# Optimization experiments

Hardware: AMD Instinct MI355X
Metric: run time of the kernel (lower is better)

The kernel has to match this reference:

```python
import jax, jax.numpy as jnp
import numpy as np

H = 56; W = 56; WS = 7; NW = WS * WS  # 49 tokens per window
HEADS = 8; DIM = 256; HIDDEN = 4 * DIM
SHIFT = NW // 2  # gilbert shift = 24 (shift_size > 0)
SCALE = (DIM // HEADS) ** -0.5
EPS = 1e-5


def _sgn(v):
    return -1 if v < 0 else 1 if v > 0 else 0


def _generate2d(x, y, ax, ay, bx, by, result):
    w = abs(ax + ay); h = abs(bx + by)
    dax, day = _sgn(ax), _sgn(ay); dbx, dby = _sgn(bx), _sgn(by)
    if h == 1 or w == 1:
        if h == 1:
            for _ in range(w):
                result.append((x, y)); x, y = x + dax, y + day
        elif w == 1:
            for _ in range(h):
                result.append((x, y)); x, y = x + dbx, y + dby
        return
    ax2, ay2 = ax // 2, ay // 2; bx2, by2 = bx // 2, by // 2
    w2 = abs(ax2 + ay2); h2 = abs(bx2 + by2)
    if 2 * w > 3 * h:
        if w2 % 2 and w > 2:
            ax2, ay2 = ax2 + dax, ay2 + day
        _generate2d(x, y, ax2, ay2, bx, by, result)
        _generate2d(x + ax2, y + ay2, ax - ax2, ay - ay2, bx, by, result)
    else:
        if h2 % 2 and h > 2:
            bx2, by2 = bx2 + dbx, by2 + dby
        _generate2d(x, y, bx2, by2, ax2, ay2, result)
        _generate2d(x + bx2, y + by2, ax, ay, bx - bx2, by - by2, result)
        _generate2d(x + (ax - dax) + (bx2 - dbx), y + (ay - day) + (by2 - dby),
                    -bx2, -by2, -(ax - ax2), -(ay - ay2), result)


def _gilbert2d(width, height):
    result = []
    if width >= height:
        _generate2d(0, 0, width, 0, 0, height, result)
    else:
        _generate2d(0, 0, 0, height, width, 0, result)
    return result


def _make_rel_index():
    # reverse_map[idx] = (y, x) for gilbert position idx
    path = _gilbert2d(W, H)
    rev = np.zeros((H * W, 2), dtype=np.int64)
    for i, (px, py) in enumerate(path[:H * W]):
        rev[i, 0] = py; rev[i, 1] = px
    pos = np.roll(rev, SHIFT, axis=0)  # shifted block: roll positions by ws^2//2
    n_windows = (H * W) // NW
    pos = pos[:n_windows * NW].reshape(n_windows, NW, 2)
    dh = pos[:, :, 0][:, :, None] - pos[:, :, 0][:, None, :] + (H - 1)
    dw = pos[:, :, 1][:, :, None] - pos[:, :, 1][:, None, :] + (W - 1)
    return (dh * (2 * W - 1) + dw).astype(np.int32)  # (nW, 49, 49)


def setup_inputs() -> dict:
    key = jax.random.key(0)
    ks = jax.random.split(key, 8)
    B, L, C = 32, H * W, DIM
    return {
        "x": jax.random.normal(ks[0], (B, L, C), jnp.float32),
        "qkv_w": jax.random.normal(ks[1], (C, 3 * C), jnp.float32) * 0.02,
        "qkv_b": jnp.zeros((3 * C,), jnp.float32),
        "proj_w": jax.random.normal(ks[2], (C, C), jnp.float32) * 0.02,
        "proj_b": jnp.zeros((C,), jnp.float32),
        "bias_table": jax.random.normal(ks[3], ((2 * H - 1) * (2 * W - 1), HEADS), jnp.float32) * 0.02,
        "norm1_w": jnp.ones((C,), jnp.float32),
        "norm1_b": jnp.zeros((C,), jnp.float32),
        "norm2_w": jnp.ones((C,), jnp.float32),
        "norm2_b": jnp.zeros((C,), jnp.float32),
        "fc1_w": jax.random.normal(ks[4], (C, HIDDEN), jnp.float32) * 0.02,
        "fc1_b": jnp.zeros((HIDDEN,), jnp.float32),
        "fc2_w": jax.random.normal(ks[5], (HIDDEN, C), jnp.float32) * 0.02,
        "fc2_b": jnp.zeros((C,), jnp.float32),
        "rel_index": jnp.asarray(_make_rel_index()),
    }


def _layernorm(x, w, b):
    mu = jnp.mean(x, axis=-1, keepdims=True)
    var = jnp.mean(jnp.square(x - mu), axis=-1, keepdims=True)
    return (x - mu) * jax.lax.rsqrt(var + EPS) * w + b


def reference(x, qkv_w, qkv_b, proj_w, proj_b, bias_table,
              norm1_w, norm1_b, norm2_w, norm2_b,
              fc1_w, fc1_b, fc2_w, fc2_b, rel_index):
    B, L, C = x.shape
    n_win = L // NW
    hd = C // HEADS

    shortcut = x
    h = _layernorm(x, norm1_w, norm1_b)
    # gilbert forward shift along the curve, then window partition
    h = jnp.roll(h, SHIFT, axis=1)
    hw = h.reshape(B * n_win, NW, C)

    qkv = (hw @ qkv_w + qkv_b).reshape(B * n_win, NW, 3, HEADS, hd)
    qkv = jnp.transpose(qkv, (2, 0, 3, 1, 4))  # (3, B*nW, heads, N, hd)
    q, k, v = qkv[0] * SCALE, qkv[1], qkv[2]

    attn = jnp.einsum('bhnd,bhmd->bhnm', q, k)  # (B*nW, heads, 49, 49)
    bias = jnp.transpose(bias_table[rel_index], (0, 3, 1, 2))  # (nW, heads, 49, 49)
    attn = attn.reshape(B, n_win, HEADS, NW, NW) + bias[None]
    attn = jax.nn.softmax(attn, axis=-1).reshape(B * n_win, HEADS, NW, NW)

    out = jnp.einsum('bhnm,bhmd->bhnd', attn, v)
    out = jnp.transpose(out, (0, 2, 1, 3)).reshape(B * n_win, NW, C)
    out = out @ proj_w + proj_b

    # window merge + gilbert reverse shift
    out = out.reshape(B, L, C)
    out = jnp.roll(out, -SHIFT, axis=1)

    x = shortcut + out
    h2 = _layernorm(x, norm2_w, norm2_b)
    h2 = jax.nn.gelu(h2 @ fc1_w + fc1_b, approximate=False) @ fc2_w + fc2_b
    return x + h2
```

## Files before the change

### kernel.cpp

```cpp
#include <hip/hip_runtime.h>
#include <math.h>

typedef unsigned short u16;
typedef __attribute__((ext_vector_type(8))) short bfrag;
typedef __attribute__((ext_vector_type(4))) float f32x4;
typedef __attribute__((ext_vector_type(4))) unsigned short us4;

#define B_SZ 32
#define L_SZ 3136
#define C_SZ 256
#define NHEADS 8
#define HID_SZ 1024
#define NW 49
#define NWIN 64
#define SHIFT 24
#define M_SZ (B_SZ * L_SZ)
#define SCALEF 0.17677669529663687f

__device__ __forceinline__ float bf2f(u16 u) {
  union { unsigned int i; float f; } v; v.i = ((unsigned)u) << 16; return v.f;
}
__device__ __forceinline__ u16 f2bf(float f) {
  union { unsigned int i; float f; } v; v.f = f;
  return (u16)((v.i + 0x7fffu + ((v.i >> 16) & 1u)) >> 16);
}
__device__ __forceinline__ void gload_lds16(const u16* g, u16* l) {
  __builtin_amdgcn_global_load_lds(
      (const __attribute__((address_space(1))) unsigned int*)g,
      (__attribute__((address_space(3))) unsigned int*)l, 16, 0, 0);
}

__global__ void transpose_kernel(const float* __restrict__ in, u16* __restrict__ out,
                                 int K, int N) {
  const int idx = blockIdx.x * 256 + threadIdx.x;
  if (idx >= K * N) return;
  const int n = idx / K;
  const int k = idx - n * K;
  out[idx] = f2bf(in[(size_t)k * N + n]);
}

__global__ void bias_kernel(const float* __restrict__ tab, const int* __restrict__ rel,
                            float* __restrict__ bm) {
  const int idx = blockIdx.x * 256 + threadIdx.x;
  const int tot = NWIN * NHEADS * NW * NW;
  if (idx >= tot) return;
  const int w = idx / (NHEADS * NW * NW);
  const int r = idx - w * (NHEADS * NW * NW);
  const int h = r / (NW * NW);
  const int ij = r - h * (NW * NW);
  bm[idx] = tab[(size_t)rel[w * NW * NW + ij] * NHEADS + h];
}

__global__ __launch_bounds__(256) void ln1_kernel(
    const float* __restrict__ x, const float* __restrict__ w,
    const float* __restrict__ b, u16* __restrict__ out) {
  const int wv = threadIdx.x >> 6;
  const int lane = threadIdx.x & 63;
  const int row0 = blockIdx.x * 16 + wv * 4;
  float4 u[4];
#pragma unroll
  for (int r = 0; r < 4; ++r)
    u[r] = *((const float4*)x + (size_t)(row0 + r) * 64 + lane);
  float s[4], sq[4];
#pragma unroll
  for (int r = 0; r < 4; ++r) {
    s[r]  = u[r].x + u[r].y + u[r].z + u[r].w;
    sq[r] = u[r].x * u[r].x + u[r].y * u[r].y + u[r].z * u[r].z + u[r].w * u[r].w;
  }
#pragma unroll
  for (int d = 1; d < 64; d <<= 1)
#pragma unroll
    for (int r = 0; r < 4; ++r) {
      s[r] += __shfl_xor(s[r], d); sq[r] += __shfl_xor(sq[r], d);
    }
  float wv4[4], bv4[4];
#pragma unroll
  for (int j = 0; j < 4; ++j) { wv4[j] = w[lane * 4 + j]; bv4[j] = b[lane * 4 + j]; }
#pragma unroll
  for (int r = 0; r < 4; ++r) {
    const int row = row0 + r;
    const float mu = s[r] * (1.0f / C_SZ);
    const float rs = rsqrtf(sq[r] * (1.0f / C_SZ) - mu * mu + 1e-5f);
    const int bb = row / L_SZ;
    int l2 = row - bb * L_SZ + SHIFT;
    if (l2 >= L_SZ) l2 -= L_SZ;
    const float vv[4] = {u[r].x, u[r].y, u[r].z, u[r].w};
    us4 ov;
#pragma unroll
    for (int j = 0; j < 4; ++j) ov[j] = f2bf((vv[j] - mu) * rs * wv4[j] + bv4[j]);
    *(us4*)(out + ((size_t)bb * L_SZ + l2) * C_SZ + lane * 4) = ov;
  }
}

__global__ __launch_bounds__(256) void ln2_kernel(
    const u16* __restrict__ x, const float* __restrict__ w,
    const float* __restrict__ b, u16* __restrict__ out) {
  const int wv = threadIdx.x >> 6;
  const int lane = threadIdx.x & 63;
  const int row0 = blockIdx.x * 16 + wv * 4;
  us4 u[4];
#pragma unroll
  for (int r = 0; r < 4; ++r)
    u[r] = *(const us4*)(x + (size_t)(row0 + r) * C_SZ + lane * 4);
  float v[4][4], s[4], sq[4];
#pragma unroll
  for (int r = 0; r < 4; ++r) {
    s[r] = 0.f; sq[r] = 0.f;
#pragma unroll
    for (int j = 0; j < 4; ++j) {
      v[r][j] = bf2f(u[r][j]); s[r] += v[r][j]; sq[r] += v[r][j] * v[r][j];
    }
  }
#pragma unroll
  for (int d = 1; d < 64; d <<= 1)
#pragma unroll
    for (int r = 0; r < 4; ++r) {
      s[r] += __shfl_xor(s[r], d); sq[r] += __shfl_xor(sq[r], d);
    }
  float wv4[4], bv4[4];
#pragma unroll
  for (int j = 0; j < 4; ++j) { wv4[j] = w[lane * 4 + j]; bv4[j] = b[lane * 4 + j]; }
#pragma unroll
  for (int r = 0; r < 4; ++r) {
    const float mu = s[r] * (1.0f / C_SZ);
    const float rs = rsqrtf(sq[r] * (1.0f / C_SZ) - mu * mu + 1e-5f);
    us4 ov;
#pragma unroll
    for (int j = 0; j < 4; ++j) ov[j] = f2bf((v[r][j] - mu) * rs * wv4[j] + bv4[j]);
    *(us4*)(out + (size_t)(row0 + r) * C_SZ + lane * 4) = ov;
  }
}

#define BM 128
#define BN 128
#define BKT 64

template <int MODE>
__global__ __launch_bounds__(256, 4) void gemm_kernel(
    const u16* __restrict__ A, const u16* __restrict__ Bt,
    const float* __restrict__ bias, int N, int K, void* __restrict__ Cout,
    const float* __restrict__ resx, const u16* __restrict__ resb2) {
  __shared__ u16 Als[BM * BKT];
  __shared__ u16 Bls[BN * BKT];
  const int nbx = N / BN;
  const int per = gridDim.x >> 3;
  const int lin = (blockIdx.x & 7) * per + (blockIdx.x >> 3);
  const int by = lin / nbx;
  const int bx = lin - by * nbx;
  const int m0 = by * BM;
  const int n0 = bx * BN;

  const int tid = threadIdx.x;
  const int lane = tid & 63;
  const int lr = lane & 15;
  const int lg = lane >> 4;
  const int wid = tid >> 6;
  const int wm = (wid >> 1) * 64;
  const int wn = (wid & 1) * 64;

  const int grow = lane >> 3;
  const int gch = (lane & 7) ^ grow;

  const f32x4 fzero = {0.f, 0.f, 0.f, 0.f};
  f32x4 acc[4][4];
#pragma unroll
  for (int i = 0; i < 4; ++i)
#pragma unroll
    for (int j = 0; j < 4; ++j) acc[i][j] = fzero;

  const u16* Agl = A + (size_t)m0 * K + gch * 8;
  const u16* Bgl = Bt + (size_t)n0 * K + gch * 8;

  for (int k0 = 0; k0 < K; k0 += BKT) {
#pragma unroll
    for (int g = 0; g < 4; ++g) {
      const int rbase = wid * 32 + g * 8;
      gload_lds16(Agl + (size_t)(rbase + grow) * K + k0, Als + rbase * 64);
      gload_lds16(Bgl + (size_t)(rbase + grow) * K + k0, Bls + rbase * 64);
    }
    __syncthreads();
#pragma unroll
    for (int s = 0; s < 2; ++s) {
      const int kg = s * 4 + lg;
      bfrag af[4], bfv[4];
#pragma unroll
      for (int m = 0; m < 4; ++m) {
        const int r = wm + m * 16 + lr;
        af[m] = *(const bfrag*)(Als + r * 64 + ((kg ^ (r & 7)) * 8));
      }
#pragma unroll
      for (int n = 0; n < 4; ++n) {
        const int r = wn + n * 16 + lr;
        bfv[n] = *(const bfrag*)(Bls + r * 64 + ((kg ^ (r & 7)) * 8));
      }
#pragma unroll
      for (int m = 0; m < 4; ++m)
#pragma unroll
        for (int n = 0; n < 4; ++n)
          acc[m][n] = __builtin_amdgcn_mfma_f32_16x16x32_bf16(af[m], bfv[n],
                                                              acc[m][n], 0, 0, 0);
    }
    __syncthreads();
  }

  float bv4[4];
#pragma unroll
  for (int n = 0; n < 4; ++n) bv4[n] = bias[n0 + wn + n * 16 + lr];

#pragma unroll
  for (int m = 0; m < 4; ++m) {
#pragma unroll
    for (int i = 0; i < 4; ++i) {
      const int row = m0 + wm + m * 16 + lg * 4 + i;
      if (MODE == 1) {
        const int bb = row / L_SZ;
        int l2 = row - bb * L_SZ - SHIFT;
        if (l2 < 0) l2 += L_SZ;
        const size_t orow = (size_t)bb * L_SZ + l2;
#pragma unroll
        for (int n = 0; n < 4; ++n) {
          const int col = n0 + wn + n * 16 + lr;
          ((u16*)Cout)[orow * N + col] =
              f2bf(resx[orow * N + col] + acc[m][n][i] + bv4[n]);
        }
      } else if (MODE == 2) {
#pragma unroll
        for (int n = 0; n < 4; ++n) {
          const int col = n0 + wn + n * 16 + lr;
          float v = acc[m][n][i] + bv4[n];
          v = 0.5f * v * (1.0f + erff(v * 0.70710678f));
          ((u16*)Cout)[(size_t)row * N + col] = f2bf(v);
        }
      } else if (MODE == 3) {
#pragma unroll
        for (int n = 0; n < 4; ++n) {
          const int col = n0 + wn + n * 16 + lr;
          ((float*)Cout)[(size_t)row * N + col] =
              acc[m][n][i] + bv4[n] + bf2f(resb2[(size_t)row * N + col]);
        }
      } else {
#pragma unroll
        for (int n = 0; n < 4; ++n) {
          const int col = n0 + wn + n * 16 + lr;
          ((u16*)Cout)[(size_t)row * N + col] = f2bf(acc[m][n][i] + bv4[n]);
        }
      }
    }
  }
}

__global__ __launch_bounds__(256) void attn_kernel(const u16* __restrict__ qkv,
                                                   const float* __restrict__ bm,
                                                   u16* __restrict__ out, int widx0) {
  __shared__ u16 Pls[4][64 * 72];
  __shared__ u16 Vls[4][64 * 32];
  const int wl = blockIdx.x >> 1;
  const int half = blockIdx.x & 1;
  const int w = (widx0 + wl) & (NWIN - 1);
  const int wv = threadIdx.x >> 6;
  const int lane = threadIdx.x & 63;
  const int lr = lane & 15;
  const int lg = lane >> 4;
  const size_t base = (size_t)wl * NW;
  u16* P = Pls[wv];
  u16* Vl = Vls[wv];
  const f32x4 fzero = {0.f, 0.f, 0.f, 0.f};
  const int h = half * 4 + wv;

#pragma unroll
  for (int g = 0; g < 4; ++g) {
    int row = g * 16 + (lane >> 2);
    if (row > NW - 1) row = NW - 1;
    const int sc = (lane & 3) ^ ((row ^ (row >> 2)) & 3);
    gload_lds16(qkv + (base + row) * 768 + 512 + h * 32 + sc * 8, Vl + g * 512);
  }

  bfrag qf[4], kf[4];
#pragma unroll
  for (int m = 0; m < 4; ++m) {
    int r = m * 16 + lr; if (r > NW - 1) r = NW - 1;
    qf[m] = *(const bfrag*)(qkv + (base + r) * 768 + h * 32 + lg * 8);
    kf[m] = *(const bfrag*)(qkv + (base + r) * 768 + 256 + h * 32 + lg * 8);
  }
  f32x4 s[4][4];
#pragma unroll
  for (int m = 0; m < 4; ++m)
#pragma unroll
    for (int n = 0; n < 4; ++n)
      s[m][n] = __builtin_amdgcn_mfma_f32_16x16x32_bf16(qf[m], kf[n], fzero, 0, 0, 0);

  const float* bh = bm + (size_t)(w * NHEADS + h) * (NW * NW);
#pragma unroll
  for (int m = 0; m < 4; ++m) {
#pragma unroll
    for (int i = 0; i < 4; ++i) {
      const int row = m * 16 + lg * 4 + i;
      const int brow = row > NW - 1 ? NW - 1 : row;
      float vals[4];
#pragma unroll
      for (int n = 0; n < 4; ++n) {
        const int c = n * 16 + lr;
        vals[n] = (c < NW) ? (s[m][n][i] * SCALEF + bh[brow * NW + c]) : -1e30f;
      }
      float mx = fmaxf(fmaxf(vals[0], vals[1]), fmaxf(vals[2], vals[3]));
#pragma unroll
      for (int d = 1; d < 16; d <<= 1) mx = fmaxf(mx, __shfl_xor(mx, d));
      float sum = 0.f;
#pragma unroll
      for (int n = 0; n < 4; ++n) { vals[n] = __expf(vals[n] - mx); sum += vals[n]; }
#pragma unroll
      for (int d = 1; d < 16; d <<= 1) sum += __shfl_xor(sum, d);
      const float inv = 1.0f / sum;
#pragma unroll
      for (int n = 0; n < 4; ++n)
        P[row * 72 + n * 16 + lr] = f2bf(vals[n] * inv);
    }
  }
  asm volatile("s_waitcnt vmcnt(0)" ::: "memory");
  f32x4 o[4][2];
#pragma unroll
  for (int m = 0; m < 4; ++m) { o[m][0] = fzero; o[m][1] = fzero; }
#pragma unroll
  for (int s2 = 0; s2 < 2; ++s2) {
    bfrag pf[4], vf[2];
#pragma unroll
    for (int m = 0; m < 4; ++m)
      pf[m] = *(const bfrag*)(P + (m * 16 + lr) * 72 + s2 * 32 + lg * 8);
#pragma unroll
    for (int n = 0; n < 2; ++n) {
      const int d = n * 16 + lr;
      const int cd = d >> 3;
#pragma unroll
      for (int i = 0; i < 8; ++i) {
        const int kk = s2 * 32 + lg * 8 + i;
        const int slot = cd ^ ((kk ^ (kk >> 2)) & 3);
        vf[n][i] = *(const short*)(Vl + kk * 32 + slot * 8 + (d & 7));
      }
    }
#pragma unroll
    for (int m = 0; m < 4; ++m)
#pragma unroll
      for (int n = 0; n < 2; ++n)
        o[m][n] = __builtin_amdgcn_mfma_f32_16x16x32_bf16(pf[m], vf[n],
                                                          o[m][n], 0, 0, 0);
  }
#pragma unroll
  for (int m = 0; m < 4; ++m)
#pragma unroll
    for (int i = 0; i < 4; ++i) {
      const int row = m * 16 + lg * 4 + i;
      if (row < NW) {
#pragma unroll
        for (int n = 0; n < 2; ++n)
          out[(base + row) * C_SZ + h * 32 + n * 16 + lr] = f2bf(o[m][n][i]);
      }
    }
}

extern "C" void kernel_launch(void* const* d_in, const int* in_sizes, int n_in,
                              void* d_out, int out_size, void* d_ws, size_t ws_size,
                              hipStream_t stream) {
  (void)in_sizes; (void)n_in; (void)out_size;
  const float* x     = (const float*)d_in[0];
  const float* qkvw  = (const float*)d_in[1];
  const float* qkvb  = (const float*)d_in[2];
  const float* projw = (const float*)d_in[3];
  const float* projb = (const float*)d_in[4];
  const float* btab  = (const float*)d_in[5];
  const float* n1w   = (const float*)d_in[6];
  const float* n1b   = (const float*)d_in[7];
  const float* n2w   = (const float*)d_in[8];
  const float* n2b   = (const float*)d_in[9];
  const float* fc1w  = (const float*)d_in[10];
  const float* fc1b  = (const float*)d_in[11];
  const float* fc2w  = (const float*)d_in[12];
  const float* fc2b  = (const float*)d_in[13];
  const int* rel     = (const int*)d_in[14];

  char* ws = (char*)d_ws;
  size_t off = 0;
  auto alloc = [&](size_t bytes) -> char* {
    char* p = ws + off; off += (bytes + 255) & ~(size_t)255; return p;
  };
  u16* qkvwT   = (u16*)alloc((size_t)768 * 256 * 2);
  u16* projwT  = (u16*)alloc((size_t)256 * 256 * 2);
  u16* fc1wT   = (u16*)alloc((size_t)1024 * 256 * 2);
  u16* fc2wT   = (u16*)alloc((size_t)256 * 1024 * 2);
  float* biasm = (float*)alloc((size_t)NWIN * NHEADS * NW * NW * 4);
  u16* bufh    = (u16*)alloc((size_t)M_SZ * C_SZ * 2);
  u16* x2b     = (u16*)alloc((size_t)M_SZ * C_SZ * 2);

  const size_t scr_chunk = (size_t)(M_SZ / 2) * HID_SZ * 2;
  const int nch = (ws_size >= off + scr_chunk) ? 2 : 4;
  const int mch = M_SZ / nch;
  const int wch = (B_SZ * NWIN) / nch;
  char* tail = ws + off;
  u16* qkvbuf   = (u16*)tail;
  u16* scratch2 = (u16*)tail;

  transpose_kernel<<<(256 * 768 + 255) / 256, 256, 0, stream>>>(qkvw, qkvwT, 256, 768);
  transpose_kernel<<<(256 * 256 + 255) / 256, 256, 0, stream>>>(projw, projwT, 256, 256);
  transpose_kernel<<<(256 * 1024 + 255) / 256, 256, 0, stream>>>(fc1w, fc1wT, 256, 1024);
  transpose_kernel<<<(1024 * 256 + 255) / 256, 256, 0, stream>>>(fc2w, fc2wT, 1024, 256);
  bias_kernel<<<(NWIN * NHEADS * NW * NW + 255) / 256, 256, 0, stream>>>(btab, rel, biasm);

  ln1_kernel<<<M_SZ / 16, 256, 0, stream>>>(x, n1w, n1b, bufh);

  for (int c = 0; c < nch; ++c) {
    const size_t roff = (size_t)c * mch;
    gemm_kernel<0><<<(768 / BN) * (mch / BM), 256, 0, stream>>>(
        bufh + roff * C_SZ, qkvwT, qkvb, 768, 256, qkvbuf, nullptr, nullptr);
    attn_kernel<<<wch * 2, 256, 0, stream>>>(qkvbuf, biasm, bufh + roff * C_SZ,
                                             c * wch);
  }

  gemm_kernel<1><<<(256 / BN) * (M_SZ / BM), 256, 0, stream>>>(
      bufh, projwT, projb, 256, 256, x2b, x, nullptr);

  for (int q = 0; q < nch; ++q) {
    const size_t roff = (size_t)q * mch;
    ln2_kernel<<<mch / 16, 256, 0, stream>>>(x2b + roff * C_SZ, n2w, n2b,
                                             bufh + roff * C_SZ);
    gemm_kernel<2><<<(HID_SZ / BN) * (mch / BM), 256, 0, stream>>>(
        bufh + roff * C_SZ, fc1wT, fc1b, 1024, 256, scratch2, nullptr, nullptr);
    gemm_kernel<3><<<(256 / BN) * (mch / BM), 256, 0, stream>>>(
        scratch2, fc2wT, fc2b, 256, 1024, (float*)d_out + roff * C_SZ,
        nullptr, x2b + roff * C_SZ);
  }
}
```

Before: 458.2 us.

## Add double-buffered 256x256-tile GEMM for MLP and process MLP unchunked

Adds a 512-thread GEMM kernel that computes 256x256 output tiles. It double-buffers the A and B tiles in LDS with swizzled direct-to-LDS loads, and is used for the fc1 (GELU) and fc2 (residual) GEMMs. When the workspace can hold the full hidden activation, the MLP now runs as a single chunk rather than two or four, and the QKV/attention loop is fixed at two chunks. The goal is more operand reuse per tile, load latency overlapped with MFMA work, and fewer launches. In exchange the new kernel uses about 128KB of LDS and a large accumulator set, so it fits only one block per CU. The fc2 grid is also small relative to the CU count, which risks tail imbalance.

```diff
diff --git a/kernel.cpp b/kernel.cpp
--- a/kernel.cpp
+++ b/kernel.cpp
@@ -139,7 +139,7 @@
 __global__ __launch_bounds__(256, 4) void gemm_kernel(
     const u16* __restrict__ A, const u16* __restrict__ Bt,
     const float* __restrict__ bias, int N, int K, void* __restrict__ Cout,
-    const float* __restrict__ resx, const u16* __restrict__ resb2) {
+    const float* __restrict__ resx) {
   __shared__ u16 Als[BM * BKT];
   __shared__ u16 Bls[BN * BKT];
   const int nbx = N / BN;
@@ -223,26 +223,120 @@
           ((u16*)Cout)[orow * N + col] =
               f2bf(resx[orow * N + col] + acc[m][n][i] + bv4[n]);
         }
-      } else if (MODE == 2) {
+      } else {
 #pragma unroll
         for (int n = 0; n < 4; ++n) {
           const int col = n0 + wn + n * 16 + lr;
+          ((u16*)Cout)[(size_t)row * N + col] = f2bf(acc[m][n][i] + bv4[n]);
+        }
+      }
+    }
+  }
+}
+
+template <int MODE>
+__global__ __launch_bounds__(512, 2) void gemm256_kernel(
+    const u16* __restrict__ A, const u16* __restrict__ Bt,
+    const float* __restrict__ bias, int N, int K, void* __restrict__ Cout,
+    const u16* __restrict__ resb2) {
+  __shared__ u16 Als[2][256 * 64];
+  __shared__ u16 Bls[2][256 * 64];
+  const int nbx = N / 256;
+  int lin;
+  if ((gridDim.x & 7) == 0) {
+    const int per = gridDim.x >> 3;
+    lin = (blockIdx.x & 7) * per + (blockIdx.x >> 3);
+  } else {
+    lin = blockIdx.x;
+  }
+  const int by = lin / nbx;
+  const int bx = lin - by * nbx;
+  const int m0 = by * 256;
+  const int n0 = bx * 256;
+
+  const int tid = threadIdx.x;
+  const int lane = tid & 63;
+  const int lr = lane & 15;
+  const int lg = lane >> 4;
+  const int wid = tid >> 6;
+  const int wr = wid >> 2;
+  const int wc = wid & 3;
+  const int grow = lane >> 3;
+  const int gch = (lane & 7) ^ grow;
+
+  const f32x4 fzero = {0.f, 0.f, 0.f, 0.f};
+  f32x4 acc[8][4];
+#pragma unroll
+  for (int m = 0; m < 8; ++m)
+#pragma unroll
+    for (int n = 0; n < 4; ++n) acc[m][n] = fzero;
+
+  const u16* Agl = A + (size_t)m0 * K + gch * 8;
+  const u16* Bgl = Bt + (size_t)n0 * K + gch * 8;
+
+  auto stage = [&](int buf, int k0) {
+#pragma unroll
+    for (int g = 0; g < 4; ++g) {
+      const int rb = wid * 32 + g * 8;
+      gload_lds16(Agl + (size_t)(rb + grow) * K + k0, Als[buf] + rb * 64);
+      gload_lds16(Bgl + (size_t)(rb + grow) * K + k0, Bls[buf] + rb * 64);
+    }
+  };
+
+  const int nk = K / 64;
+  stage(0, 0);
+  __syncthreads();
+  int cur = 0;
+  for (int kb = 0; kb < nk; ++kb) {
+    if (kb + 1 < nk) stage(cur ^ 1, (kb + 1) * 64);
+#pragma unroll
+    for (int s = 0; s < 2; ++s) {
+      const int kg = s * 4 + lg;
+      bfrag af[8], bfv[4];
+#pragma unroll
+      for (int m = 0; m < 8; ++m) {
+        const int r = wr * 128 + m * 16 + lr;
+        af[m] = *(const bfrag*)(Als[cur] + r * 64 + ((kg ^ (r & 7)) * 8));
+      }
+#pragma unroll
+      for (int n = 0; n < 4; ++n) {
+        const int r = wc * 64 + n * 16 + lr;
+        bfv[n] = *(const bfrag*)(Bls[cur] + r * 64 + ((kg ^ (r & 7)) * 8));
+      }
+#pragma unroll
+      for (int m = 0; m < 8; ++m)
+#pragma unroll
+        for (int n = 0; n < 4; ++n)
+          acc[m][n] = __builtin_amdgcn_mfma_f32_16x16x32_bf16(af[m], bfv[n],
+                                                              acc[m][n], 0, 0, 0);
+    }
+    __syncthreads();
+    cur ^= 1;
+  }
+
+  float bv4[4];
+#pragma unroll
+  for (int n = 0; n < 4; ++n) bv4[n] = bias[n0 + wc * 64 + n * 16 + lr];
+
+#pragma unroll
+  for (int m = 0; m < 8; ++m) {
+#pragma unroll
+    for (int i = 0; i < 4; ++i) {
+      const int row = m0 + wr * 128 + m * 16 + lg * 4 + i;
+      if (MODE == 2) {
+#pragma unroll
+        for (int n = 0; n < 4; ++n) {
+          const int col = n0 + wc * 64 + n * 16 + lr;
           float v = acc[m][n][i] + bv4[n];
           v = 0.5f * v * (1.0f + erff(v * 0.70710678f));
           ((u16*)Cout)[(size_t)row * N + col] = f2bf(v);
         }
-      } else if (MODE == 3) {
+      } else {
 #pragma unroll
         for (int n = 0; n < 4; ++n) {
-          const int col = n0 + wn + n * 16 + lr;
+          const int col = n0 + wc * 64 + n * 16 + lr;
           ((float*)Cout)[(size_t)row * N + col] =
               acc[m][n][i] + bv4[n] + bf2f(resb2[(size_t)row * N + col]);
-        }
-      } else {
-#pragma unroll
-        for (int n = 0; n < 4; ++n) {
-          const int col = n0 + wn + n * 16 + lr;
-          ((u16*)Cout)[(size_t)row * N + col] = f2bf(acc[m][n][i] + bv4[n]);
         }
       }
     }
@@ -390,10 +484,12 @@
   u16* bufh    = (u16*)alloc((size_t)M_SZ * C_SZ * 2);
   u16* x2b     = (u16*)alloc((size_t)M_SZ * C_SZ * 2);
 
-  const size_t scr_chunk = (size_t)(M_SZ / 2) * HID_SZ * 2;
-  const int nch = (ws_size >= off + scr_chunk) ? 2 : 4;
-  const int mch = M_SZ / nch;
-  const int wch = (B_SZ * NWIN) / nch;
+  const size_t full_scr = (size_t)M_SZ * HID_SZ * 2;
+  const int nch_mlp = (ws_size >= off + full_scr) ? 1 : 2;
+  const int mch_mlp = M_SZ / nch_mlp;
+  const int nch_qkv = 2;
+  const int mch = M_SZ / nch_qkv;
+  const int wch = (B_SZ * NWIN) / nch_qkv;
   char* tail = ws + off;
   u16* qkvbuf   = (u16*)tail;
   u16* scratch2 = (u16*)tail;
@@ -406,25 +502,25 @@
 
   ln1_kernel<<<M_SZ / 16, 256, 0, stream>>>(x, n1w, n1b, bufh);
 
-  for (int c = 0; c < nch; ++c) {
+  for (int c = 0; c < nch_qkv; ++c) {
     const size_t roff = (size_t)c * mch;
     gemm_kernel<0><<<(768 / BN) * (mch / BM), 256, 0, stream>>>(
-        bufh + roff * C_SZ, qkvwT, qkvb, 768, 256, qkvbuf, nullptr, nullptr);
+        bufh + roff * C_SZ, qkvwT, qkvb, 768, 256, qkvbuf, nullptr);
     attn_kernel<<<wch * 2, 256, 0, stream>>>(qkvbuf, biasm, bufh + roff * C_SZ,
                                              c * wch);
   }
 
   gemm_kernel<1><<<(256 / BN) * (M_SZ / BM), 256, 0, stream>>>(
-      bufh, projwT, projb, 256, 256, x2b, x, nullptr);
-
-  for (int q = 0; q < nch; ++q) {
-    const size_t roff = (size_t)q * mch;
-    ln2_kernel<<<mch / 16, 256, 0, stream>>>(x2b + roff * C_SZ, n2w, n2b,
-                                             bufh + roff * C_SZ);
-    gemm_kernel<2><<<(HID_SZ / BN) * (mch / BM), 256, 0, stream>>>(
-        bufh + roff * C_SZ, fc1wT, fc1b, 1024, 256, scratch2, nullptr, nullptr);
-    gemm_kernel<3><<<(256 / BN) * (mch / BM), 256, 0, stream>>>(
+      bufh, projwT, projb, 256, 256, x2b, x);
+
+  for (int q = 0; q < nch_mlp; ++q) {
+    const size_t roff = (size_t)q * mch_mlp;
+    ln2_kernel<<<mch_mlp / 16, 256, 0, stream>>>(x2b + roff * C_SZ, n2w, n2b,
+                                                 bufh + roff * C_SZ);
+    gemm256_kernel<2><<<(HID_SZ / 256) * (mch_mlp / 256), 512, 0, stream>>>(
+        bufh + roff * C_SZ, fc1wT, fc1b, 1024, 256, scratch2, nullptr);
+    gemm256_kernel<3><<<(256 / 256) * (mch_mlp / 256), 512, 0, stream>>>(
         scratch2, fc2wT, fc2b, 256, 1024, (float*)d_out + roff * C_SZ,
-        nullptr, x2b + roff * C_SZ);
-  }
-}
+        x2b + roff * C_SZ);
+  }
+}
```

Result: slower. 536.5 us (+17.1%).
